# Optimization experiments

Hardware: AMD Instinct MI355X
Metric: run time of the kernel (lower is better)

Reference implementation:

```python
import jax, jax.numpy as jnp
import numpy as np

B_SZ, L, D, N = 4, 2048, 768, 16


def setup_inputs() -> dict:
    key = jax.random.key(0)
    ks = jax.random.split(key, 8)
    x = jax.random.normal(ks[0], (B_SZ, L, D), dtype=jnp.float32)
    # A_log initialized as log(arange(1..N)) repeated over d, as in the module
    A_log = jnp.log(jnp.broadcast_to(jnp.arange(1, N + 1, dtype=jnp.float32), (D, N)))
    # s_b_c: Linear(D, 2N)
    W_bc = jax.random.normal(ks[1], (2 * N, D), dtype=jnp.float32) / jnp.sqrt(D)
    b_bc = jnp.zeros((2 * N,), dtype=jnp.float32)
    # s_1: Linear(D, 1)
    W_1 = jax.random.normal(ks[2], (1, D), dtype=jnp.float32) / jnp.sqrt(D)
    b_1 = jnp.zeros((1,), dtype=jnp.float32)
    # s_delta: Linear(1, D)
    W_d = jax.random.normal(ks[3], (D, 1), dtype=jnp.float32)
    b_d = jnp.zeros((D,), dtype=jnp.float32)
    return {"x": x, "A_log": A_log, "W_bc": W_bc, "b_bc": b_bc,
            "W_1": W_1, "b_1": b_1, "W_d": W_d, "b_d": b_d}


def reference(x, A_log, W_bc, b_bc, W_1, b_1, W_d, b_d):
    b, l, d = x.shape
    n = A_log.shape[1]
    A = -jnp.exp(A_log)                                   # (d, n)
    BandC = x @ W_bc.T + b_bc                             # (b, l, 2n)
    Bm, Cm = BandC[..., :n], BandC[..., n:]               # (b, l, n) each
    # delta = softplus(s_delta(s_1(x)))  -> (b, l, d)
    s1 = x @ W_1.T + b_1                                  # (b, l, 1)
    delta = jax.nn.softplus(s1 @ W_d.T + b_d)             # (b, l, d)
    deltaA = jnp.exp(jnp.einsum('bld,dn->bldn', delta, A))        # (b, l, d, n)
    deltaB_u = jnp.einsum('bld,bln,bld->bldn', delta, Bm, x)      # (b, l, d, n)

    # sequential selective-scan over time with lax.scan
    dA_t = jnp.moveaxis(deltaA, 1, 0)      # (l, b, d, n)
    dBu_t = jnp.moveaxis(deltaB_u, 1, 0)   # (l, b, d, n)
    C_t = jnp.moveaxis(Cm, 1, 0)           # (l, b, n)

    def step(h, inp):
        dA_i, dBu_i, c_i = inp
        h = dA_i * h + dBu_i               # (b, d, n)
        y = jnp.einsum('bdn,bn->bd', h, c_i)
        return h, y

    h0 = jnp.zeros((b, d, n), dtype=x.dtype)
    _, ys = jax.lax.scan(step, h0, (dA_t, dBu_t, C_t))
    return jnp.moveaxis(ys, 0, 1)          # (b, l, d)
```

## Files before the change

kernel.cpp:

```cpp
#include <hip/hip_runtime.h>

#define L_SEQ 2048
#define D_DIM 768
#define N_ST 16
#define NB 4
#define NJ 33
#define BCS 48
#define NROWS (NB * L_SEQ)
#define PROJ_ELEMS (NROWS * NJ)
#define DN (D_DIM * N_ST)

#define DSPLIT 8
#define DSEG (D_DIM / DSPLIT)
#define DK 32
#define NCHUNK (DSEG / DK)
#define RB 128
#define XST 132
#define WST 64

typedef float v2f __attribute__((ext_vector_type(2)));

__device__ __forceinline__ float fast_exp2(float x) {
#if __has_builtin(__builtin_amdgcn_exp2f)
  return __builtin_amdgcn_exp2f(x);
#else
  return __expf(x * 0.69314718055994531f);
#endif
}

__device__ __forceinline__ float softplus_f(float v) {
  float e = fast_exp2(v * 1.44269504088896f);
  float l = __log2f(1.0f + e) * 0.69314718055994531f;
  return (v > 15.0f) ? v : l;
}

__device__ __forceinline__ void pow_tree2(float e1, v2f pw2[8]) {
  float e2s = e1 * e1;
  float e4s = e2s * e2s;
  float e8s = e4s * e4s;
  v2f s2 = {e2s, e2s}, s4 = {e4s, e4s}, s8 = {e8s, e8s};
  pw2[0] = (v2f){e1, e2s};
  pw2[1] = pw2[0] * s2;
  pw2[2] = pw2[0] * s4;
  pw2[3] = pw2[1] * s4;
  pw2[4] = pw2[0] * s8;
  pw2[5] = pw2[1] * s8;
  pw2[6] = pw2[2] * s8;
  pw2[7] = pw2[3] * s8;
}

__global__ __launch_bounds__(256) void k_proj_gemm(
    const float* __restrict__ x, const float* __restrict__ W_bc,
    const float* __restrict__ W_1, float* __restrict__ PBC) {
  __shared__ float xs_t[DK * XST];
  __shared__ float ws_t[DK * WST];

  const int ds  = blockIdx.x % DSPLIT;
  const int rb0 = (blockIdx.x / DSPLIT) * RB;
  const int dbase = ds * DSEG;
  const int tid = threadIdx.x;
  const int rg = tid & 31;
  const int jg = tid >> 5;

  float acc[4][5];
#pragma unroll
  for (int i = 0; i < 4; ++i)
#pragma unroll
    for (int k = 0; k < 5; ++k) acc[i][k] = 0.0f;

  const int lrow = tid >> 1;
  const int lhalf = (tid & 1) * 16;
  const float* xg_row = x + (size_t)(rb0 + lrow) * D_DIM + dbase + lhalf;

  for (int ch = 0; ch < NCHUNK; ++ch) {
    const int dc = dbase + ch * DK;
    float4 xv[4];
#pragma unroll
    for (int q = 0; q < 4; ++q)
      xv[q] = *(const float4*)(xg_row + ch * DK + q * 4);
    float wv[8];
    int widx[8];
#pragma unroll
    for (int u = 0; u < 8; ++u) {
      int idx = tid + u * 256;
      int dk = idx >> 6, slot = idx & 63;
      int wjg = slot >> 3, wk = slot & 7;
      int j = wjg + 8 * wk;
      float v = 0.0f;
      if (wk < 5) {
        if (j < 32)       v = W_bc[(size_t)j * D_DIM + dc + dk];
        else if (j == 32) v = W_1[dc + dk];
      }
      wv[u] = v; widx[u] = dk * WST + slot;
    }
    __syncthreads();
#pragma unroll
    for (int q = 0; q < 4; ++q) {
      xs_t[(lhalf + q * 4 + 0) * XST + lrow] = xv[q].x;
      xs_t[(lhalf + q * 4 + 1) * XST + lrow] = xv[q].y;
      xs_t[(lhalf + q * 4 + 2) * XST + lrow] = xv[q].z;
      xs_t[(lhalf + q * 4 + 3) * XST + lrow] = xv[q].w;
    }
#pragma unroll
    for (int u = 0; u < 8; ++u) ws_t[widx[u]] = wv[u];
    __syncthreads();
#pragma unroll 8
    for (int dk = 0; dk < DK; ++dk) {
      float4 xr = *(const float4*)&xs_t[dk * XST + rg * 4];
      float4 wr = *(const float4*)&ws_t[dk * WST + jg * 8];
      float w4  = ws_t[dk * WST + jg * 8 + 4];
      float xa[4] = {xr.x, xr.y, xr.z, xr.w};
      float wa[5] = {wr.x, wr.y, wr.z, wr.w, w4};
#pragma unroll
      for (int i = 0; i < 4; ++i)
#pragma unroll
        for (int k = 0; k < 5; ++k)
          acc[i][k] = fmaf(xa[i], wa[k], acc[i][k]);
    }
  }

  float* pb = PBC + (size_t)ds * PROJ_ELEMS;
#pragma unroll
  for (int i = 0; i < 4; ++i) {
    int row = rb0 + rg * 4 + i;
#pragma unroll
    for (int k = 0; k < 5; ++k) {
      int j = jg + 8 * k;
      if (k < 4 || jg == 0) pb[(size_t)row * NJ + j] = acc[i][k];
    }
  }
}

__global__ __launch_bounds__(256) void k_proj_reduce(
    const float* __restrict__ PBC, const float* __restrict__ b_bc,
    const float* __restrict__ b_1, float* __restrict__ BC48) {
  const int idx = blockIdx.x * 256 + threadIdx.x;
  const int row = idx / NJ;
  const int j = idx - row * NJ;
  float s = 0.0f;
#pragma unroll
  for (int k = 0; k < DSPLIT; ++k) s += PBC[(size_t)k * PROJ_ELEMS + idx];
  s += (j < 32) ? b_bc[j] : b_1[0];
  BC48[(size_t)row * BCS + j] = s;
}

template <int LC>
__global__ __launch_bounds__(256, 6) void k_scan1(
    const float* __restrict__ x, const float* __restrict__ A_log,
    const float* __restrict__ W_d, const float* __restrict__ b_d,
    const float* __restrict__ BC48, float* __restrict__ DS,
    float* __restrict__ H, int NC) {
  const int cb = blockIdx.x % 3;
  const int c  = (blockIdx.x / 3) % NC;
  const int b  = blockIdx.x / (3 * NC);
  const int d  = cb * 256 + threadIdx.x;

  const float wd = W_d[d], bd = b_d[d];
  float Aln[N_ST];
  {
    const float4* al4 = (const float4*)(A_log + (size_t)d * N_ST);
#pragma unroll
    for (int q = 0; q < 4; ++q) {
      float4 v = al4[q];
      Aln[4*q+0] = -__expf(v.x) * 1.44269504088896f;
      Aln[4*q+1] = -__expf(v.y) * 1.44269504088896f;
      Aln[4*q+2] = -__expf(v.z) * 1.44269504088896f;
      Aln[4*q+3] = -__expf(v.w) * 1.44269504088896f;
    }
  }
  bool geom = true;
#pragma unroll
  for (int n = 1; n < N_ST; ++n) {
    float ref = (float)(n + 1) * Aln[0];
    geom = geom && (fabsf(Aln[n] - ref) <= 1e-4f * fabsf(ref) + 1e-12f);
  }
  const float a0 = Aln[0];

  v2f h2[8];
#pragma unroll
  for (int k = 0; k < 8; ++k) h2[k] = (v2f){0.0f, 0.0f};
  float dsum = 0.0f;

  const int l0 = c * LC;
  const float* bc = BC48 + (size_t)(b * L_SEQ + l0) * BCS;
  const float* xp = x + (size_t)(b * L_SEQ + l0) * D_DIM + d;

  if (geom) {
#pragma unroll 8
    for (int l = 0; l < LC; ++l) {
      const float* r = bc + l * BCS;
      float4 B0 = *(const float4*)(r + 0);
      float4 B1 = *(const float4*)(r + 4);
      float4 B2 = *(const float4*)(r + 8);
      float4 B3 = *(const float4*)(r + 12);
      float s1 = r[32];
      float delta = softplus_f(fmaf(s1, wd, bd));
      float xv = xp[(size_t)l * D_DIM];
      float f = delta * xv;
      dsum += delta;
      v2f pw2[8];
      pow_tree2(fast_exp2(a0 * delta), pw2);
      v2f f2 = {f, f};
      h2[0] = pw2[0] * h2[0] + f2 * (v2f){B0.x, B0.y};
      h2[1] = pw2[1] * h2[1] + f2 * (v2f){B0.z, B0.w};
      h2[2] = pw2[2] * h2[2] + f2 * (v2f){B1.x, B1.y};
      h2[3] = pw2[3] * h2[3] + f2 * (v2f){B1.z, B1.w};
      h2[4] = pw2[4] * h2[4] + f2 * (v2f){B2.x, B2.y};
      h2[5] = pw2[5] * h2[5] + f2 * (v2f){B2.z, B2.w};
      h2[6] = pw2[6] * h2[6] + f2 * (v2f){B3.x, B3.y};
      h2[7] = pw2[7] * h2[7] + f2 * (v2f){B3.z, B3.w};
    }
  } else {
#pragma unroll 4
    for (int l = 0; l < LC; ++l) {
      const float* r = bc + l * BCS;
      float s1 = r[32];
      float delta = softplus_f(fmaf(s1, wd, bd));
      float f = delta * xp[(size_t)l * D_DIM];
      dsum += delta;
#pragma unroll
      for (int k = 0; k < 8; ++k) {
        h2[k].x = fmaf(fast_exp2(delta * Aln[2*k]),   h2[k].x, f * r[2*k]);
        h2[k].y = fmaf(fast_exp2(delta * Aln[2*k+1]), h2[k].y, f * r[2*k+1]);
      }
    }
  }

  DS[((size_t)b * NC + c) * D_DIM + d] = dsum;
  size_t base = ((size_t)(b * NC + c) * D_DIM + d) * N_ST;
  float4* H4 = (float4*)(H + base);
#pragma unroll
  for (int q = 0; q < 4; ++q)
    H4[q] = make_float4(h2[2*q].x, h2[2*q].y, h2[2*q+1].x, h2[2*q+1].y);
}

template <int SC>
__global__ __launch_bounds__(256) void k_combine_par(
    const float* __restrict__ A_log, const float* __restrict__ DS,
    float* __restrict__ H, int NC) {
  __shared__ float Pl[8 * 33];
  __shared__ float Hl[8 * 33];
  const int b    = blockIdx.x / 384;
  const int dn0  = (blockIdx.x % 384) * 32;
  const int lane = threadIdx.x & 31;
  const int j    = threadIdx.x >> 5;
  const int dn   = dn0 + lane;
  const int d    = dn >> 4;

  const float Aln1 = -__expf(A_log[dn]) * 1.44269504088896f;

  const float* dsp = DS + (size_t)b * NC * D_DIM + d;
  float* Hp = H + (size_t)b * NC * DN + dn;

  float p[SC], ph[SC];
#pragma unroll
  for (int k = 0; k < SC; ++k) {
    const int c = j * SC + k;
    p[k]  = fast_exp2(Aln1 * dsp[(size_t)c * D_DIM]);
    ph[k] = Hp[(size_t)c * DN];
  }

  float Pagg = 1.0f, Hagg = 0.0f;
#pragma unroll
  for (int k = 0; k < SC; ++k) {
    Hagg = fmaf(p[k], Hagg, ph[k]);
    Pagg *= p[k];
  }

  Pl[j * 33 + lane] = Pagg;
  Hl[j * 33 + lane] = Hagg;
  __syncthreads();

  float h = 0.0f;
  for (int j2 = 0; j2 < j; ++j2)
    h = fmaf(Pl[j2 * 33 + lane], h, Hl[j2 * 33 + lane]);

#pragma unroll
  for (int k = 0; k < SC; ++k) {
    Hp[(size_t)(j * SC + k) * DN] = h;
    h = fmaf(p[k], h, ph[k]);
  }
}

template <int LC>
__global__ __launch_bounds__(256, 6) void k_scan2(
    const float* __restrict__ x, const float* __restrict__ A_log,
    const float* __restrict__ W_d, const float* __restrict__ b_d,
    const float* __restrict__ BC48, const float* __restrict__ HIN,
    float* __restrict__ out, int NC) {
  const int cb = blockIdx.x % 3;
  const int c  = (blockIdx.x / 3) % NC;
  const int b  = blockIdx.x / (3 * NC);
  const int d  = cb * 256 + threadIdx.x;

  const float wd = W_d[d], bd = b_d[d];
  float Aln[N_ST];
  {
    const float4* al4 = (const float4*)(A_log + (size_t)d * N_ST);
#pragma unroll
    for (int q = 0; q < 4; ++q) {
      float4 v = al4[q];
      Aln[4*q+0] = -__expf(v.x) * 1.44269504088896f;
      Aln[4*q+1] = -__expf(v.y) * 1.44269504088896f;
      Aln[4*q+2] = -__expf(v.z) * 1.44269504088896f;
      Aln[4*q+3] = -__expf(v.w) * 1.44269504088896f;
    }
  }
  bool geom = true;
#pragma unroll
  for (int n = 1; n < N_ST; ++n) {
    float ref = (float)(n + 1) * Aln[0];
    geom = geom && (fabsf(Aln[n] - ref) <= 1e-4f * fabsf(ref) + 1e-12f);
  }
  const float a0 = Aln[0];

  v2f h2[8];
  {
    size_t base = ((size_t)(b * NC + c) * D_DIM + d) * N_ST;
    const float4* HIN4 = (const float4*)(HIN + base);
#pragma unroll
    for (int q = 0; q < 4; ++q) {
      float4 v = HIN4[q];
      h2[2*q]   = (v2f){v.x, v.y};
      h2[2*q+1] = (v2f){v.z, v.w};
    }
  }

  const int l0 = c * LC;
  const float* bc = BC48 + (size_t)(b * L_SEQ + l0) * BCS;
  const float* xp = x + (size_t)(b * L_SEQ + l0) * D_DIM + d;
  float* op = out + (size_t)(b * L_SEQ + l0) * D_DIM + d;

  if (geom) {
#pragma unroll 8
    for (int l = 0; l < LC; ++l) {
      const float* r = bc + l * BCS;
      float4 B0 = *(const float4*)(r + 0);
      float4 B1 = *(const float4*)(r + 4);
      float4 B2 = *(const float4*)(r + 8);
      float4 B3 = *(const float4*)(r + 12);
      float4 C0 = *(const float4*)(r + 16);
      float4 C1 = *(const float4*)(r + 20);
      float4 C2 = *(const float4*)(r + 24);
      float4 C3 = *(const float4*)(r + 28);
      float s1 = r[32];
      float delta = softplus_f(fmaf(s1, wd, bd));
      float xv = xp[(size_t)l * D_DIM];
      float f = delta * xv;
      v2f pw2[8];
      pow_tree2(fast_exp2(a0 * delta), pw2);
      v2f f2 = {f, f};
      v2f y2 = {0.0f, 0.0f};
      h2[0] = pw2[0] * h2[0] + f2 * (v2f){B0.x, B0.y};  y2 += h2[0] * (v2f){C0.x, C0.y};
      h2[1] = pw2[1] * h2[1] + f2 * (v2f){B0.z, B0.w};  y2 += h2[1] * (v2f){C0.z, C0.w};
      h2[2] = pw2[2] * h2[2] + f2 * (v2f){B1.x, B1.y};  y2 += h2[2] * (v2f){C1.x, C1.y};
      h2[3] = pw2[3] * h2[3] + f2 * (v2f){B1.z, B1.w};  y2 += h2[3] * (v2f){C1.z, C1.w};
      h2[4] = pw2[4] * h2[4] + f2 * (v2f){B2.x, B2.y};  y2 += h2[4] * (v2f){C2.x, C2.y};
      h2[5] = pw2[5] * h2[5] + f2 * (v2f){B2.z, B2.w};  y2 += h2[5] * (v2f){C2.z, C2.w};
      h2[6] = pw2[6] * h2[6] + f2 * (v2f){B3.x, B3.y};  y2 += h2[6] * (v2f){C3.x, C3.y};
      h2[7] = pw2[7] * h2[7] + f2 * (v2f){B3.z, B3.w};  y2 += h2[7] * (v2f){C3.z, C3.w};
      op[(size_t)l * D_DIM] = y2.x + y2.y;
    }
  } else {
#pragma unroll 4
    for (int l = 0; l < LC; ++l) {
      const float* r = bc + l * BCS;
      float s1 = r[32];
      float delta = softplus_f(fmaf(s1, wd, bd));
      float f = delta * xp[(size_t)l * D_DIM];
      float y = 0.0f;
#pragma unroll
      for (int k = 0; k < 8; ++k) {
        h2[k].x = fmaf(fast_exp2(delta * Aln[2*k]),   h2[k].x, f * r[2*k]);
        h2[k].y = fmaf(fast_exp2(delta * Aln[2*k+1]), h2[k].y, f * r[2*k+1]);
        y = fmaf(h2[k].x, r[16 + 2*k], y);
        y = fmaf(h2[k].y, r[16 + 2*k + 1], y);
      }
      op[(size_t)l * D_DIM] = y;
    }
  }
}

extern "C" void kernel_launch(void* const* d_in, const int* in_sizes, int n_in,
                              void* d_out, int out_size, void* d_ws, size_t ws_size,
                              hipStream_t stream) {
  const float* x     = (const float*)d_in[0];
  const float* A_log = (const float*)d_in[1];
  const float* W_bc  = (const float*)d_in[2];
  const float* b_bc  = (const float*)d_in[3];
  const float* W_1   = (const float*)d_in[4];
  const float* b_1   = (const float*)d_in[5];
  const float* W_d   = (const float*)d_in[6];
  const float* b_d   = (const float*)d_in[7];
  float* out = (float*)d_out;
  float* ws  = (float*)d_ws;

  int NC = 128;
  {
    size_t need = ((size_t)NROWS * BCS + 8ull * PROJ_ELEMS +
                   (3072ull + 49152ull) * 128) * 4ull;
    if (ws_size < need) NC = 64;
  }

  float* BC48 = ws;
  float* PBC  = ws + (size_t)NROWS * BCS;
  float* DSb  = PBC + (size_t)DSPLIT * PROJ_ELEMS;
  float* H    = DSb + (size_t)3072 * NC;

  k_proj_gemm<<<(NROWS / RB) * DSPLIT, 256, 0, stream>>>(x, W_bc, W_1, PBC);
  k_proj_reduce<<<(PROJ_ELEMS + 255) / 256, 256, 0, stream>>>(PBC, b_bc, b_1, BC48);

  const int gs = 3 * NB * NC;
  if (NC == 128) {
    k_scan1<16><<<gs, 256, 0, stream>>>(x, A_log, W_d, b_d, BC48, DSb, H, NC);
    k_combine_par<16><<<NB * 384, 256, 0, stream>>>(A_log, DSb, H, NC);
    k_scan2<16><<<gs, 256, 0, stream>>>(x, A_log, W_d, b_d, BC48, H, out, NC);
  } else {
    k_scan1<32><<<gs, 256, 0, stream>>>(x, A_log, W_d, b_d, BC48, DSb, H, NC);
    k_combine_par<8><<<NB * 384, 256, 0, stream>>>(A_log, DSb, H, NC);
    k_scan2<32><<<gs, 256, 0, stream>>>(x, A_log, W_d, b_d, BC48, H, out, NC);
  }
}
```

Measured before the change: 151.2 us.

## Fuse reduce, scan and combine phases into one cooperative kernel with grid syncs

Merges the projection reduce, chunk scan, cross-chunk combine and output scan into one persistent cooperative kernel of 768 blocks, separated by grid.sync(). It also fixes the chunk count at 64 (chunk length 32) and reshapes the combine phase to 64 lanes by 4 segments. The aim is to remove the launch overhead and inter-kernel gaps between the four launches. In exchange it pays for grid-wide barriers, caps occupancy at 3 blocks per SM and halves chunk-level parallelism compared with the previous 128-chunk path. A fallback to separate launches remains if cooperative launch is unavailable.

Result: no change. 151.6 us (+0.3%).

```diff
diff --git a/kernel.cpp b/kernel.cpp
--- a/kernel.cpp
+++ b/kernel.cpp
@@ -1,4 +1,7 @@
 #include <hip/hip_runtime.h>
+#include <hip/hip_cooperative_groups.h>
+
+namespace cg = cooperative_groups;
 
 #define L_SEQ 2048
 #define D_DIM 768
@@ -9,6 +12,12 @@
 #define NROWS (NB * L_SEQ)
 #define PROJ_ELEMS (NROWS * NJ)
 #define DN (D_DIM * N_ST)
+
+#define NCC 64
+#define LCC 32
+#define GS  768
+#define SEGC 4
+#define SCC 16
 
 #define DSPLIT 8
 #define DSEG (D_DIM / DSPLIT)
@@ -131,28 +140,29 @@
   }
 }
 
-__global__ __launch_bounds__(256) void k_proj_reduce(
+__device__ __forceinline__ void phase_reduce(
     const float* __restrict__ PBC, const float* __restrict__ b_bc,
     const float* __restrict__ b_1, float* __restrict__ BC48) {
-  const int idx = blockIdx.x * 256 + threadIdx.x;
-  const int row = idx / NJ;
-  const int j = idx - row * NJ;
-  float s = 0.0f;
-#pragma unroll
-  for (int k = 0; k < DSPLIT; ++k) s += PBC[(size_t)k * PROJ_ELEMS + idx];
-  s += (j < 32) ? b_bc[j] : b_1[0];
-  BC48[(size_t)row * BCS + j] = s;
-}
-
-template <int LC>
-__global__ __launch_bounds__(256, 6) void k_scan1(
+  const int t0 = blockIdx.x * 256 + threadIdx.x;
+  for (int idx = t0; idx < PROJ_ELEMS; idx += GS * 256) {
+    const int row = idx / NJ;
+    const int j = idx - row * NJ;
+    float s = 0.0f;
+#pragma unroll
+    for (int k = 0; k < DSPLIT; ++k) s += PBC[(size_t)k * PROJ_ELEMS + idx];
+    s += (j < 32) ? b_bc[j] : b_1[0];
+    BC48[(size_t)row * BCS + j] = s;
+  }
+}
+
+__device__ __forceinline__ void phase_scan1(
     const float* __restrict__ x, const float* __restrict__ A_log,
     const float* __restrict__ W_d, const float* __restrict__ b_d,
     const float* __restrict__ BC48, float* __restrict__ DS,
-    float* __restrict__ H, int NC) {
+    float* __restrict__ H) {
   const int cb = blockIdx.x % 3;
-  const int c  = (blockIdx.x / 3) % NC;
-  const int b  = blockIdx.x / (3 * NC);
+  const int c  = (blockIdx.x / 3) % NCC;
+  const int b  = blockIdx.x / (3 * NCC);
   const int d  = cb * 256 + threadIdx.x;
 
   const float wd = W_d[d], bd = b_d[d];
@@ -181,13 +191,13 @@
   for (int k = 0; k < 8; ++k) h2[k] = (v2f){0.0f, 0.0f};
   float dsum = 0.0f;
 
-  const int l0 = c * LC;
+  const int l0 = c * LCC;
   const float* bc = BC48 + (size_t)(b * L_SEQ + l0) * BCS;
   const float* xp = x + (size_t)(b * L_SEQ + l0) * D_DIM + d;
 
   if (geom) {
 #pragma unroll 8
-    for (int l = 0; l < LC; ++l) {
+    for (int l = 0; l < LCC; ++l) {
       const float* r = bc + l * BCS;
       float4 B0 = *(const float4*)(r + 0);
       float4 B1 = *(const float4*)(r + 4);
@@ -212,7 +222,7 @@
     }
   } else {
 #pragma unroll 4
-    for (int l = 0; l < LC; ++l) {
+    for (int l = 0; l < LCC; ++l) {
       const float* r = bc + l * BCS;
       float s1 = r[32];
       float delta = softplus_f(fmaf(s1, wd, bd));
@@ -226,71 +236,69 @@
     }
   }
 
-  DS[((size_t)b * NC + c) * D_DIM + d] = dsum;
-  size_t base = ((size_t)(b * NC + c) * D_DIM + d) * N_ST;
+  DS[((size_t)b * NCC + c) * D_DIM + d] = dsum;
+  size_t base = ((size_t)(b * NCC + c) * D_DIM + d) * N_ST;
   float4* H4 = (float4*)(H + base);
 #pragma unroll
   for (int q = 0; q < 4; ++q)
     H4[q] = make_float4(h2[2*q].x, h2[2*q].y, h2[2*q+1].x, h2[2*q+1].y);
 }
 
-template <int SC>
-__global__ __launch_bounds__(256) void k_combine_par(
+__device__ __forceinline__ void phase_combine(
     const float* __restrict__ A_log, const float* __restrict__ DS,
-    float* __restrict__ H, int NC) {
-  __shared__ float Pl[8 * 33];
-  __shared__ float Hl[8 * 33];
-  const int b    = blockIdx.x / 384;
-  const int dn0  = (blockIdx.x % 384) * 32;
-  const int lane = threadIdx.x & 31;
-  const int j    = threadIdx.x >> 5;
+    float* __restrict__ H) {
+  __shared__ float Pl[SEGC * 65];
+  __shared__ float Hl[SEGC * 65];
+  const int b    = blockIdx.x / 192;
+  const int dn0  = (blockIdx.x % 192) * 64;
+  const int lane = threadIdx.x & 63;
+  const int j    = threadIdx.x >> 6;
   const int dn   = dn0 + lane;
   const int d    = dn >> 4;
 
   const float Aln1 = -__expf(A_log[dn]) * 1.44269504088896f;
 
-  const float* dsp = DS + (size_t)b * NC * D_DIM + d;
-  float* Hp = H + (size_t)b * NC * DN + dn;
-
-  float p[SC], ph[SC];
-#pragma unroll
-  for (int k = 0; k < SC; ++k) {
-    const int c = j * SC + k;
+  const float* dsp = DS + (size_t)b * NCC * D_DIM + d;
+  float* Hp = H + (size_t)b * NCC * DN + dn;
+
+  float p[SCC], ph[SCC];
+#pragma unroll
+  for (int k = 0; k < SCC; ++k) {
+    const int c = j * SCC + k;
     p[k]  = fast_exp2(Aln1 * dsp[(size_t)c * D_DIM]);
     ph[k] = Hp[(size_t)c * DN];
   }
 
   float Pagg = 1.0f, Hagg = 0.0f;
 #pragma unroll
-  for (int k = 0; k < SC; ++k) {
+  for (int k = 0; k < SCC; ++k) {
     Hagg = fmaf(p[k], Hagg, ph[k]);
     Pagg *= p[k];
   }
 
-  Pl[j * 33 + lane] = Pagg;
-  Hl[j * 33 + lane] = Hagg;
+  Pl[j * 65 + lane] = Pagg;
+  Hl[j * 65 + lane] = Hagg;
   __syncthreads();
 
   float h = 0.0f;
   for (int j2 = 0; j2 < j; ++j2)
-    h = fmaf(Pl[j2 * 33 + lane], h, Hl[j2 * 33 + lane]);
-
-#pragma unroll
-  for (int k = 0; k < SC; ++k) {
-    Hp[(size_t)(j * SC + k) * DN] = h;
+    h = fmaf(Pl[j2 * 65 + lane], h, Hl[j2 * 65 + lane]);
+
+#pragma unroll
+  for (int k = 0; k < SCC; ++k) {
+    Hp[(size_t)(j * SCC + k) * DN] = h;
     h = fmaf(p[k], h, ph[k]);
   }
 }
 
-template <int LC>
-__global__ __launch_bounds__(256, 6) void k_scan2(
+__device__ __forceinline__ void phase_scan2(
     const float* __restrict__ x, const float* __restrict__ A_log,
     const float* __restrict__ W_d, const float* __restrict__ b_d,
     const float* __restrict__ BC48, const float* __restrict__ HIN,
-    float* __restrict__ out, int NC) {
+    float* __restrict__ out) {
   const int cb = blockIdx.x % 3;
-  const int c  = (blockIdx.x / 3) % NC;
-  const int b  = blockIdx.x / (3 * NC);
+  const int c  = (blockIdx.x / 3) % NCC;
+  const int b  = blockIdx.x / (3 * NCC);
   const int d  = cb * 256 + threadIdx.x;
 
   const float wd = W_d[d], bd = b_d[d];
@@ -316,7 +324,7 @@
 
   v2f h2[8];
   {
-    size_t base = ((size_t)(b * NC + c) * D_DIM + d) * N_ST;
+    size_t base = ((size_t)(b * NCC + c) * D_DIM + d) * N_ST;
     const float4* HIN4 = (const float4*)(HIN + base);
 #pragma unroll
     for (int q = 0; q < 4; ++q) {
@@ -326,14 +334,14 @@
     }
   }
 
-  const int l0 = c * LC;
+  const int l0 = c * LCC;
   const float* bc = BC48 + (size_t)(b * L_SEQ + l0) * BCS;
   const float* xp = x + (size_t)(b * L_SEQ + l0) * D_DIM + d;
   float* op = out + (size_t)(b * L_SEQ + l0) * D_DIM + d;
 
   if (geom) {
 #pragma unroll 8
-    for (int l = 0; l < LC; ++l) {
+    for (int l = 0; l < LCC; ++l) {
       const float* r = bc + l * BCS;
       float4 B0 = *(const float4*)(r + 0);
       float4 B1 = *(const float4*)(r + 4);
@@ -363,7 +371,7 @@
     }
   } else {
 #pragma unroll 4
-    for (int l = 0; l < LC; ++l) {
+    for (int l = 0; l < LCC; ++l) {
       const float* r = bc + l * BCS;
       float s1 = r[32];
       float delta = softplus_f(fmaf(s1, wd, bd));
@@ -379,6 +387,47 @@
       op[(size_t)l * D_DIM] = y;
     }
   }
+}
+
+__global__ __launch_bounds__(256, 3) void k_mega(
+    const float* __restrict__ x, const float* __restrict__ A_log,
+    const float* __restrict__ W_d, const float* __restrict__ b_d,
+    const float* __restrict__ PBC, const float* __restrict__ b_bc,
+    const float* __restrict__ b_1, float* __restrict__ BC48,
+    float* __restrict__ DS, float* __restrict__ H, float* __restrict__ out) {
+  cg::grid_group grid = cg::this_grid();
+  phase_reduce(PBC, b_bc, b_1, BC48);
+  grid.sync();
+  phase_scan1(x, A_log, W_d, b_d, BC48, DS, H);
+  grid.sync();
+  phase_combine(A_log, DS, H);
+  grid.sync();
+  phase_scan2(x, A_log, W_d, b_d, BC48, H, out);
+}
+
+__global__ __launch_bounds__(256) void k_reduce_f(
+    const float* __restrict__ PBC, const float* __restrict__ b_bc,
+    const float* __restrict__ b_1, float* __restrict__ BC48) {
+  phase_reduce(PBC, b_bc, b_1, BC48);
+}
+__global__ __launch_bounds__(256, 3) void k_scan1_f(
+    const float* __restrict__ x, const float* __restrict__ A_log,
+    const float* __restrict__ W_d, const float* __restrict__ b_d,
+    const float* __restrict__ BC48, float* __restrict__ DS,
+    float* __restrict__ H) {
+  phase_scan1(x, A_log, W_d, b_d, BC48, DS, H);
+}
+__global__ __launch_bounds__(256) void k_combine_f(
+    const float* __restrict__ A_log, const float* __restrict__ DS,
+    float* __restrict__ H) {
+  phase_combine(A_log, DS, H);
+}
+__global__ __launch_bounds__(256, 3) void k_scan2_f(
+    const float* __restrict__ x, const float* __restrict__ A_log,
+    const float* __restrict__ W_d, const float* __restrict__ b_d,
+    const float* __restrict__ BC48, const float* __restrict__ HIN,
+    float* __restrict__ out) {
+  phase_scan2(x, A_log, W_d, b_d, BC48, HIN, out);
 }
 
 extern "C" void kernel_launch(void* const* d_in, const int* in_sizes, int n_in,
@@ -395,29 +444,34 @@
   float* out = (float*)d_out;
   float* ws  = (float*)d_ws;
 
-  int NC = 128;
-  {
-    size_t need = ((size_t)NROWS * BCS + 8ull * PROJ_ELEMS +
-                   (3072ull + 49152ull) * 128) * 4ull;
-    if (ws_size < need) NC = 64;
-  }
-
   float* BC48 = ws;
-  float* PBC  = ws + (size_t)NROWS * BCS;
+  float* PBC  = BC48 + (size_t)NROWS * BCS;
   float* DSb  = PBC + (size_t)DSPLIT * PROJ_ELEMS;
-  float* H    = DSb + (size_t)3072 * NC;
+  float* H    = DSb + (size_t)NB * NCC * D_DIM;
 
   k_proj_gemm<<<(NROWS / RB) * DSPLIT, 256, 0, stream>>>(x, W_bc, W_1, PBC);
-  k_proj_reduce<<<(PROJ_ELEMS + 255) / 256, 256, 0, stream>>>(PBC, b_bc, b_1, BC48);
-
-  const int gs = 3 * NB * NC;
-  if (NC == 128) {
-    k_scan1<16><<<gs, 256, 0, stream>>>(x, A_log, W_d, b_d, BC48, DSb, H, NC);
-    k_combine_par<16><<<NB * 384, 256, 0, stream>>>(A_log, DSb, H, NC);
-    k_scan2<16><<<gs, 256, 0, stream>>>(x, A_log, W_d, b_d, BC48, H, out, NC);
-  } else {
-    k_scan1<32><<<gs, 256, 0, stream>>>(x, A_log, W_d, b_d, BC48, DSb, H, NC);
-    k_combine_par<8><<<NB * 384, 256, 0, stream>>>(A_log, DSb, H, NC);
-    k_scan2<32><<<gs, 256, 0, stream>>>(x, A_log, W_d, b_d, BC48, H, out, NC);
-  }
-}
+
+  static int coop = -1;
+  if (coop < 0) {
+    int dev = 0;
+    (void)hipGetDevice(&dev);
+    int v = 0;
+    (void)hipDeviceGetAttribute(&v, hipDeviceAttributeCooperativeLaunch, dev);
+    coop = v ? 1 : 0;
+  }
+
+  if (coop == 1) {
+    void* args[] = {(void*)&x, (void*)&A_log, (void*)&W_d, (void*)&b_d,
+                    (void*)&PBC, (void*)&b_bc, (void*)&b_1,
+                    (void*)&BC48, (void*)&DSb, (void*)&H, (void*)&out};
+    hipError_t e = hipLaunchCooperativeKernel((const void*)k_mega, dim3(GS),
+                                              dim3(256), args, 0, stream);
+    if (e == hipSuccess) return;
+    coop = 0;
+  }
+
+  k_reduce_f<<<GS, 256, 0, stream>>>(PBC, b_bc, b_1, BC48);
+  k_scan1_f<<<GS, 256, 0, stream>>>(x, A_log, W_d, b_d, BC48, DSb, H);
+  k_combine_f<<<GS, 256, 0, stream>>>(A_log, DSb, H);
+  k_scan2_f<<<GS, 256, 0, stream>>>(x, A_log, W_d, b_d, BC48, H, out);
+}
```
